# Kernel optimization log

Hardware: AMD Instinct MI355X
Metric: run time of the kernel (lower is better)

## Reference

```python
import jax, jax.numpy as jnp
import numpy as np

B, S, H, C = 8, 4096, 768, 64  # batch, seq_len, hidden_dim, block size


def _xavier(k, shape):
    fan = shape[0] + shape[1]
    return jax.random.normal(k, shape, jnp.float32) * np.sqrt(2.0 / fan)


def setup_inputs() -> dict:
    key = jax.random.key(0)
    kx, kq, kk, kv, k1, k2 = jax.random.split(key, 6)
    return {
        "x": jax.random.normal(kx, (B, S, H), jnp.float32),
        "Wq": _xavier(kq, (H, H)),
        "Wk": _xavier(kk, (H, H)),
        "Wv": _xavier(kv, (H, H)),
        "W1": _xavier(k1, (H, 16)),
        "W2": _xavier(k2, (16, H)),
        "b": jnp.zeros((H,), jnp.float32),
    }


def reference(x, Wq, Wk, Wv, W1, W2, b):
    Bb, Ss, Hh = x.shape
    NB = Ss // C  # number of blocks (seq_len divisible by C, no remainder)
    Q = x @ Wq
    K = x @ Wk
    V = x @ Wv
    # gating alpha: identical every block iteration in the original, compute once
    alpha = jax.nn.sigmoid((x @ W1) @ W2 + b) ** (1.0 / 16.0)  # [B,S,H]
    a = alpha.mean(axis=1, keepdims=True)  # [B,1,H], broadcasts over rows of state
    # blocks to leading axis for scan: [NB, B, C, H]
    qs = Q.reshape(Bb, NB, C, Hh).transpose(1, 0, 2, 3)
    ks = K.reshape(Bb, NB, C, Hh).transpose(1, 0, 2, 3)
    vs = V.reshape(Bb, NB, C, Hh).transpose(1, 0, 2, 3)
    mask = jnp.tril(jnp.ones((C, C), x.dtype))
    scale = 1.0 / np.sqrt(Hh).astype(np.float32)

    def step(St, blk):
        qb, kb, vb = blk  # each [B,C,H]
        # state update first (original updates S before computing output)
        St = St * a + jnp.einsum("bch,bcd->bhd", kb, vb)  # [B,H,H]
        # intra-block: scores masked by MULTIPLICATION (as in original), then softmax
        scores = jnp.einsum("bch,bdh->bcd", qb, kb) * mask * scale
        w = jax.nn.softmax(scores, axis=-1)
        out = jnp.einsum("bch,bhd->bcd", qb, St) + jnp.einsum("bcd,bde->bce", w, vb)
        return St, out

    S0 = jnp.zeros((Bb, Hh, Hh), x.dtype)
    _, outs = jax.lax.scan(step, S0, (qs, ks, vs))  # outs: [NB,B,C,H]
    O = outs.transpose(1, 0, 2, 3).reshape(Bb, Ss, Hh)
    return O
```

## Files before the change

kernel.cpp:

```cpp
#include <hip/hip_runtime.h>

#define B_ 8
#define S_ 4096
#define H_ 768
#define C_ 64
#define NB_ 64
#define M_ (B_*S_)

#define NCH_ 8
#define LCH_ 8

typedef _Float16 f16x8 __attribute__((ext_vector_type(8)));
typedef _Float16 f16x4 __attribute__((ext_vector_type(4)));
typedef float    f32x4 __attribute__((ext_vector_type(4)));

__global__ __launch_bounds__(256) void k_transpose(const float* __restrict__ src,
                                                   _Float16* __restrict__ dst) {
  __shared__ float tile[32][33];
  const int t = threadIdx.x;
  const int tx = t & 31, ty = t >> 5;
  const int n0 = blockIdx.x * 32, k0 = blockIdx.y * 32;
#pragma unroll
  for (int i = 0; i < 4; ++i)
    tile[ty + i*8][tx] = src[(k0 + ty + i*8) * H_ + n0 + tx];
  __syncthreads();
#pragma unroll
  for (int i = 0; i < 4; ++i)
    dst[(n0 + ty + i*8) * H_ + k0 + tx] = (_Float16)tile[tx][ty + i*8];
}

__global__ __launch_bounds__(256) void k_gemm_qkv(
    const float* __restrict__ x,
    const _Float16* __restrict__ WqT, const _Float16* __restrict__ WkT,
    const _Float16* __restrict__ WvT,
    _Float16* __restrict__ Qb,
    _Float16* __restrict__ KT, _Float16* __restrict__ VT) {
  __shared__ _Float16 xs[64][40];
  __shared__ _Float16 ws[3][128][40];
  const int t = threadIdx.x;
  const int m0 = blockIdx.x * 64, n0 = blockIdx.y * 128;
  const int lane = t & 63, wv = t >> 6;
  const int lm = lane & 15, qd = lane >> 4;
  const int sm = t >> 2, sk = (t & 3) * 8;
  const int wn = t >> 1, wk = (t & 1) * 16;

  f32x4 acc[3][4][2];
#pragma unroll
  for (int a = 0; a < 3; ++a)
#pragma unroll
    for (int i = 0; i < 4; ++i)
#pragma unroll
      for (int n = 0; n < 2; ++n)
        acc[a][i][n] = (f32x4){0.f, 0.f, 0.f, 0.f};

  for (int kk = 0; kk < 24; ++kk) {
    const int k0 = kk * 32;
    __syncthreads();
    {
      const f32x4* xp = (const f32x4*)&x[(size_t)(m0 + sm) * H_ + k0 + sk];
      f32x4 f0 = xp[0], f1 = xp[1];
      f16x8 xv;
#pragma unroll
      for (int j = 0; j < 4; ++j) { xv[j] = (_Float16)f0[j]; xv[4 + j] = (_Float16)f1[j]; }
      *(f16x8*)&xs[sm][sk] = xv;
    }
    {
      const f16x8* wp = (const f16x8*)&WqT[(n0 + wn) * H_ + k0 + wk];
      *(f16x8*)&ws[0][wn][wk] = wp[0]; *(f16x8*)&ws[0][wn][wk + 8] = wp[1];
      wp = (const f16x8*)&WkT[(n0 + wn) * H_ + k0 + wk];
      *(f16x8*)&ws[1][wn][wk] = wp[0]; *(f16x8*)&ws[1][wn][wk + 8] = wp[1];
      wp = (const f16x8*)&WvT[(n0 + wn) * H_ + k0 + wk];
      *(f16x8*)&ws[2][wn][wk] = wp[0]; *(f16x8*)&ws[2][wn][wk + 8] = wp[1];
    }
    __syncthreads();
    f16x8 af[4];
#pragma unroll
    for (int i = 0; i < 4; ++i) af[i] = *(f16x8*)&xs[i*16 + lm][qd*8];
#pragma unroll
    for (int a = 0; a < 3; ++a)
#pragma unroll
      for (int n = 0; n < 2; ++n) {
        f16x8 bfr = *(f16x8*)&ws[a][wv*32 + n*16 + lm][qd*8];
#pragma unroll
        for (int i = 0; i < 4; ++i)
          acc[a][i][n] = __builtin_amdgcn_mfma_f32_16x16x32_f16(af[i], bfr, acc[a][i][n], 0, 0, 0);
      }
  }
#pragma unroll
  for (int i = 0; i < 4; ++i)
#pragma unroll
    for (int n = 0; n < 2; ++n) {
      const int ng = n0 + wv*32 + n*16 + lm;
      const int mg0 = m0 + i*16 + qd*4;
      const int bb = mg0 >> 12, ss = mg0 & (S_ - 1);
#pragma unroll
      for (int r = 0; r < 4; ++r)
        Qb[(size_t)(mg0 + r) * H_ + ng] = (_Float16)acc[0][i][n][r];
      f16x4 kp, vp;
#pragma unroll
      for (int r = 0; r < 4; ++r) {
        kp[r] = (_Float16)acc[1][i][n][r];
        vp[r] = (_Float16)acc[2][i][n][r];
      }
      *(f16x4*)&KT[((size_t)bb * H_ + ng) * S_ + ss] = kp;
      *(f16x4*)&VT[((size_t)bb * H_ + ng) * S_ + ss] = vp;
    }
}

__global__ __launch_bounds__(256) void k_tgemm(const float* __restrict__ x,
                                               const float* __restrict__ W1,
                                               float* __restrict__ tbuf) {
  __shared__ float w1s[768 * 16];
  __shared__ float xs[64 * 129];
  const int t = threadIdx.x;
  const int m0 = blockIdx.x * 64;
  for (int i = t; i < 768 * 16 / 4; i += 256)
    ((f32x4*)w1s)[i] = ((const f32x4*)W1)[i];
  const int row = t & 63, cg = t >> 6;
  f32x4 acc = (f32x4){0.f, 0.f, 0.f, 0.f};
  for (int kc = 0; kc < 768; kc += 128) {
    __syncthreads();
    for (int i = 0; i < 32; ++i) {
      const int idx = t + 256 * i;
      const int r = idx >> 7, c = idx & 127;
      xs[r * 129 + c] = x[(size_t)(m0 + r) * H_ + kc + c];
    }
    __syncthreads();
#pragma unroll 8
    for (int kl = 0; kl < 128; ++kl) {
      const float a = xs[row * 129 + kl];
      const f32x4 w = *(const f32x4*)&w1s[(kc + kl) * 16 + cg * 4];
#pragma unroll
      for (int j = 0; j < 4; ++j) acc[j] += a * w[j];
    }
  }
  *(f32x4*)&tbuf[(size_t)(m0 + row) * 16 + cg * 4] = acc;
}

__global__ __launch_bounds__(256) void k_areduce(const float* __restrict__ tbuf,
                                                 const float* __restrict__ W2,
                                                 const float* __restrict__ bias,
                                                 float* __restrict__ abuf) {
  __shared__ float ts[128 * 17];
  __shared__ float rbuf[8 * 32];
  const int t = threadIdx.x;
  const int b = blockIdx.y, hc = blockIdx.x;
  const int hl = t & 31, sg = t >> 5;
  const int h = hc * 32 + hl;
  float w2r[16];
#pragma unroll
  for (int j = 0; j < 16; ++j) w2r[j] = W2[j * H_ + h];
  const float bb = bias[h];
  float asum = 0.f;
  const float* tb = &tbuf[(size_t)(b * S_) * 16];
  for (int sc = 0; sc < S_; sc += 128) {
    __syncthreads();
    for (int i = 0; i < 8; ++i) {
      const int idx = t + 256 * i;
      const int sl = idx >> 4, j = idx & 15;
      ts[sl * 17 + j] = tb[(size_t)(sc + sl) * 16 + j];
    }
    __syncthreads();
    for (int i = 0; i < 16; ++i) {
      const int sl = sg + i * 8;
      float z = bb;
      const float* tr = &ts[sl * 17];
#pragma unroll
      for (int j = 0; j < 16; ++j) z += tr[j] * w2r[j];
      const float sgm = 1.f / (1.f + __expf(-z));
      asum += sqrtf(sqrtf(sqrtf(sqrtf(sgm))));
    }
  }
  rbuf[sg * 32 + hl] = asum;
  __syncthreads();
  if (t < 32) {
    float s = 0.f;
#pragma unroll
    for (int g = 0; g < 8; ++g) s += rbuf[g * 32 + t];
    abuf[b * H_ + hc * 32 + t] = s * (1.f / (float)S_);
  }
}

__global__ __launch_bounds__(256) void k_scores_y(
    const _Float16* __restrict__ Qb, const _Float16* __restrict__ KT,
    const _Float16* __restrict__ VT, float* __restrict__ O) {
  __shared__ float qs[64 * 68];
  __shared__ float ks[64 * 68];
  __shared__ float wb[64 * 68];
  __shared__ float vsb[64 * 68];
  const int t = threadIdx.x;
  const int nb = blockIdx.x, b = blockIdx.y;
  const size_t base = ((size_t)b * S_ + nb * 64) * H_;
  const int tc = t >> 4, td = t & 15;
  const int srow = t >> 2, sseg = (t & 3) * 16;

  float scr[4][4];
#pragma unroll
  for (int i = 0; i < 4; ++i)
#pragma unroll
    for (int u = 0; u < 4; ++u) scr[i][u] = 0.f;

  for (int hc = 0; hc < 12; ++hc) {
    __syncthreads();
    {
      const f16x8* qp = (const f16x8*)&Qb[base + (size_t)srow * H_ + hc * 64 + sseg];
      f16x8 q0 = qp[0], q1 = qp[1];
#pragma unroll
      for (int j = 0; j < 8; ++j) {
        qs[(sseg + j) * 68 + srow] = (float)q0[j];
        qs[(sseg + 8 + j) * 68 + srow] = (float)q1[j];
      }
    }
    {
      const size_t krow = ((size_t)b * H_ + hc * 64 + srow) * S_ + nb * 64 + sseg;
      f16x8 k0 = *(const f16x8*)&KT[krow];
      f16x8 k1 = *(const f16x8*)&KT[krow + 8];
      f32x4 f;
#pragma unroll
      for (int j = 0; j < 4; ++j) f[j] = (float)k0[j];
      *(f32x4*)&ks[srow * 68 + sseg] = f;
#pragma unroll
      for (int j = 0; j < 4; ++j) f[j] = (float)k0[4 + j];
      *(f32x4*)&ks[srow * 68 + sseg + 4] = f;
#pragma unroll
      for (int j = 0; j < 4; ++j) f[j] = (float)k1[j];
      *(f32x4*)&ks[srow * 68 + sseg + 8] = f;
#pragma unroll
      for (int j = 0; j < 4; ++j) f[j] = (float)k1[4 + j];
      *(f32x4*)&ks[srow * 68 + sseg + 12] = f;
    }
    __syncthreads();
#pragma unroll 4
    for (int h = 0; h < 64; ++h) {
      const f32x4 qv = *(f32x4*)&qs[h * 68 + tc * 4];
      const f32x4 kv = *(f32x4*)&ks[h * 68 + td * 4];
#pragma unroll
      for (int i = 0; i < 4; ++i)
#pragma unroll
        for (int u = 0; u < 4; ++u) scr[i][u] += qv[i] * kv[u];
    }
  }
  const float scale = 0.036084391824351615f;
#pragma unroll
  for (int i = 0; i < 4; ++i)
#pragma unroll
    for (int u = 0; u < 4; ++u) {
      const int c = tc * 4 + i, d = td * 4 + u;
      wb[d * 68 + c] = (d <= c) ? scr[i][u] * scale : 0.f;
    }
  __syncthreads();
  {
    const int r = t >> 2, g = t & 3;
    float vals[16];
    float mx = -1e30f;
#pragma unroll
    for (int i = 0; i < 16; ++i) {
      vals[i] = wb[(g * 16 + i) * 68 + r];
      mx = fmaxf(mx, vals[i]);
    }
    mx = fmaxf(mx, __shfl_xor(mx, 1));
    mx = fmaxf(mx, __shfl_xor(mx, 2));
    float sm = 0.f;
#pragma unroll
    for (int i = 0; i < 16; ++i) { vals[i] = __expf(vals[i] - mx); sm += vals[i]; }
    sm += __shfl_xor(sm, 1);
    sm += __shfl_xor(sm, 2);
    const float inv = 1.f / sm;
#pragma unroll
    for (int i = 0; i < 16; ++i) wb[(g * 16 + i) * 68 + r] = vals[i] * inv;
  }
  for (int ec = 0; ec < 12; ++ec) {
    __syncthreads();
    {
      const size_t vrow = ((size_t)b * H_ + ec * 64 + srow) * S_ + nb * 64 + sseg;
      f16x8 v0 = *(const f16x8*)&VT[vrow];
      f16x8 v1 = *(const f16x8*)&VT[vrow + 8];
#pragma unroll
      for (int j = 0; j < 8; ++j) {
        vsb[(sseg + j) * 68 + srow] = (float)v0[j];
        vsb[(sseg + 8 + j) * 68 + srow] = (float)v1[j];
      }
    }
    __syncthreads();
    float y[4][4];
#pragma unroll
    for (int i = 0; i < 4; ++i)
#pragma unroll
      for (int u = 0; u < 4; ++u) y[i][u] = 0.f;
#pragma unroll 4
    for (int j = 0; j < 64; ++j) {
      const f32x4 wv = *(f32x4*)&wb[j * 68 + tc * 4];
      const f32x4 vv = *(f32x4*)&vsb[j * 68 + td * 4];
#pragma unroll
      for (int i = 0; i < 4; ++i)
#pragma unroll
        for (int u = 0; u < 4; ++u) y[i][u] += wv[i] * vv[u];
    }
#pragma unroll
    for (int i = 0; i < 4; ++i) {
      f32x4 yv = {y[i][0], y[i][1], y[i][2], y[i][3]};
      *(f32x4*)&O[base + (size_t)(tc * 4 + i) * H_ + ec * 64 + td * 4] = yv;
    }
  }
}

__global__ __launch_bounds__(256, 2) void k_chunk_gemm(
    const _Float16* __restrict__ KT, const _Float16* __restrict__ VT,
    const float* __restrict__ abuf, _Float16* __restrict__ Tb) {
  __shared__ _Float16 bs[128][40];
  const int t = threadIdx.x;
  const int b = blockIdx.y;
  const int ch = blockIdx.x & 7, tile = blockIdx.x >> 3;
  const int dt = tile / 6, ht = tile % 6;
  const int w = t >> 6, lane = t & 63;
  const int lm = lane & 15, qd = lane >> 4;
  const int d0 = dt * 128 + w * 32;
  const int h0 = ht * 128;
  const int hrow = t >> 1, hseg = (t & 1) * 16;

  float av[2], pw[2];
  av[0] = abuf[b * H_ + d0 + lm];
  av[1] = abuf[b * H_ + d0 + 16 + lm];
  pw[0] = 1.f; pw[1] = 1.f;

  f32x4 acc[2][8];
#pragma unroll
  for (int ds = 0; ds < 2; ++ds)
#pragma unroll
    for (int hh = 0; hh < 8; ++hh) acc[ds][hh] = (f32x4){0.f, 0.f, 0.f, 0.f};

  const size_t ktb = (size_t)b * H_ * S_;
  for (int kk = 15; kk >= 0; --kk) {
    const int sp = ch * 512 + kk * 32;
    __syncthreads();
    {
      const f16x8* kp = (const f16x8*)&KT[ktb + (size_t)(h0 + hrow) * S_ + sp + hseg];
      *(f16x8*)&bs[hrow][hseg] = kp[0];
      *(f16x8*)&bs[hrow][hseg + 8] = kp[1];
    }
    __syncthreads();
    f16x8 va0 = *(const f16x8*)&VT[ktb + (size_t)(d0 + lm) * S_ + sp + qd * 8];
    f16x8 va1 = *(const f16x8*)&VT[ktb + (size_t)(d0 + 16 + lm) * S_ + sp + qd * 8];
    va0 *= (_Float16)pw[0];
    va1 *= (_Float16)pw[1];
#pragma unroll
    for (int hh = 0; hh < 8; ++hh) {
      const f16x8 kf = *(const f16x8*)&bs[hh * 16 + lm][qd * 8];
      acc[0][hh] = __builtin_amdgcn_mfma_f32_16x16x32_f16(va0, kf, acc[0][hh], 0, 0, 0);
      acc[1][hh] = __builtin_amdgcn_mfma_f32_16x16x32_f16(va1, kf, acc[1][hh], 0, 0, 0);
    }
    if (!(kk & 1)) { pw[0] *= av[0]; pw[1] *= av[1]; }
  }
  _Float16* tp = Tb + (size_t)(b * NCH_ + ch) * 768 * 768;
#pragma unroll
  for (int ds = 0; ds < 2; ++ds)
#pragma unroll
    for (int hh = 0; hh < 8; ++hh)
#pragma unroll
      for (int r = 0; r < 4; ++r)
        tp[(size_t)(d0 + ds * 16 + qd * 4 + r) * 768 + h0 + hh * 16 + lm] =
            (_Float16)acc[ds][hh][r];
}

__global__ __launch_bounds__(256) void k_combine(const float* __restrict__ abuf,
                                                 _Float16* __restrict__ Tb) {
  const int gid = blockIdx.x * 256 + threadIdx.x;
  const int hv = gid % 96;
  const int dl = (gid / 96) & 31;
  const int dt = (gid / (96 * 32)) % 24;
  const int b  = gid / (96 * 32 * 24);
  const float ad = abuf[b * H_ + dt * 32 + dl];
  const float a2 = ad * ad, a4 = a2 * a2;
  const float aL = a4 * a4;
  float carry[8];
#pragma unroll
  for (int j = 0; j < 8; ++j) carry[j] = 0.f;
  const size_t chstride = (size_t)24 * 32 * 768;
  _Float16* p = Tb + (size_t)b * NCH_ * chstride + ((size_t)dt * 32 + dl) * 768 + hv * 8;
  for (int ch = 0; ch < NCH_; ++ch, p += chstride) {
    const f16x8 tv = *(const f16x8*)p;
    f16x8 cv;
#pragma unroll
    for (int j = 0; j < 8; ++j) {
      cv[j] = (_Float16)carry[j];
      carry[j] = carry[j] * aL + (float)tv[j];
    }
    *(f16x8*)p = cv;
  }
}

#define STP 776
__global__ __launch_bounds__(256, 2) void k_scan_out(
    const _Float16* __restrict__ Qb, const _Float16* __restrict__ KT,
    const _Float16* __restrict__ VT, const float* __restrict__ abuf,
    const _Float16* __restrict__ Tb, float* __restrict__ O) {
  __shared__ _Float16 StL[32 * STP];
  const int t = threadIdx.x;
  const int lin = blockIdx.x;
  const int xcd = lin & 7, j = lin >> 3;
  const int g = (j / 24) * 8 + xcd;
  const int dt = j % 24;
  const int ch = g & 7, b = g >> 3;
  const int d0 = dt * 32;
  const int w = t >> 6, lane = t & 63;
  const int lm = lane & 15, qd = lane >> 4;

  const float av0 = abuf[b * H_ + d0 + lm];
  const float av1 = abuf[b * H_ + d0 + 16 + lm];

  f32x4 acc[12][2];
  {
    const _Float16* tp = Tb + ((((size_t)b * NCH_ + ch) * 24 + dt) * 32) * 768;
#pragma unroll
    for (int mt = 0; mt < 12; ++mt) {
      const int h = (w * 12 + mt) * 16 + qd * 4;
      const f16x4 c0 = *(const f16x4*)&tp[(size_t)lm * 768 + h];
      const f16x4 c1 = *(const f16x4*)&tp[(size_t)(16 + lm) * 768 + h];
#pragma unroll
      for (int r = 0; r < 4; ++r) {
        acc[mt][0][r] = (float)c0[r];
        acc[mt][1][r] = (float)c1[r];
      }
    }
  }

  const size_t ktb = (size_t)b * H_ * S_;
  const size_t vrow0 = ktb + (size_t)(d0 + lm) * S_;
  const size_t vrow1 = ktb + (size_t)(d0 + 16 + lm) * S_;

  for (int blk = ch * LCH_; blk < ch * LCH_ + LCH_; ++blk) {
    const int s0 = blk * 64;
    f16x8 vf00 = *(const f16x8*)&VT[vrow0 + s0 + qd * 8];
    f16x8 vf01 = *(const f16x8*)&VT[vrow0 + s0 + 32 + qd * 8];
    f16x8 vf10 = *(const f16x8*)&VT[vrow1 + s0 + qd * 8];
    f16x8 vf11 = *(const f16x8*)&VT[vrow1 + s0 + 32 + qd * 8];
#pragma unroll
    for (int mt = 0; mt < 12; ++mt) {
      const size_t arow = ktb + (size_t)((w * 12 + mt) * 16 + lm) * S_ + s0 + qd * 8;
      f16x8 a0 = *(const f16x8*)&KT[arow];
      f16x8 a1 = *(const f16x8*)&KT[arow + 32];
      f32x4 c0 = acc[mt][0] * av0;
      f32x4 c1 = acc[mt][1] * av1;
      c0 = __builtin_amdgcn_mfma_f32_16x16x32_f16(a0, vf00, c0, 0, 0, 0);
      c0 = __builtin_amdgcn_mfma_f32_16x16x32_f16(a1, vf01, c0, 0, 0, 0);
      c1 = __builtin_amdgcn_mfma_f32_16x16x32_f16(a0, vf10, c1, 0, 0, 0);
      c1 = __builtin_amdgcn_mfma_f32_16x16x32_f16(a1, vf11, c1, 0, 0, 0);
      acc[mt][0] = c0;
      acc[mt][1] = c1;
    }
    __syncthreads();
#pragma unroll
    for (int mt = 0; mt < 12; ++mt) {
      const int h = (w * 12 + mt) * 16 + qd * 4;
      f16x4 p0, p1;
#pragma unroll
      for (int r = 0; r < 4; ++r) {
        p0[r] = (_Float16)acc[mt][0][r];
        p1[r] = (_Float16)acc[mt][1][r];
      }
      *(f16x4*)&StL[lm * STP + h] = p0;
      *(f16x4*)&StL[(16 + lm) * STP + h] = p1;
    }
    __syncthreads();
    f32x4 o0a = {0.f,0.f,0.f,0.f}, o0b = {0.f,0.f,0.f,0.f};
    f32x4 o1a = {0.f,0.f,0.f,0.f}, o1b = {0.f,0.f,0.f,0.f};
    const size_t qrow = ((size_t)b * S_ + s0 + w * 16 + lm) * H_ + qd * 8;
#pragma unroll 3
    for (int kt = 0; kt < 24; kt += 2) {
      f16x8 qa = *(const f16x8*)&Qb[qrow + kt * 32];
      f16x8 qb2 = *(const f16x8*)&Qb[qrow + kt * 32 + 32];
      f16x8 s00 = *(f16x8*)&StL[lm * STP + kt * 32 + qd * 8];
      f16x8 s01 = *(f16x8*)&StL[(16 + lm) * STP + kt * 32 + qd * 8];
      f16x8 s10 = *(f16x8*)&StL[lm * STP + kt * 32 + 32 + qd * 8];
      f16x8 s11 = *(f16x8*)&StL[(16 + lm) * STP + kt * 32 + 32 + qd * 8];
      o0a = __builtin_amdgcn_mfma_f32_16x16x32_f16(qa, s00, o0a, 0, 0, 0);
      o1a = __builtin_amdgcn_mfma_f32_16x16x32_f16(qa, s01, o1a, 0, 0, 0);
      o0b = __builtin_amdgcn_mfma_f32_16x16x32_f16(qb2, s10, o0b, 0, 0, 0);
      o1b = __builtin_amdgcn_mfma_f32_16x16x32_f16(qb2, s11, o1b, 0, 0, 0);
    }
    const f32x4 o0 = o0a + o0b;
    const f32x4 o1 = o1a + o1b;
    const size_t orow = ((size_t)b * S_ + s0 + w * 16 + qd * 4) * H_ + d0;
#pragma unroll
    for (int r = 0; r < 4; ++r) {
      O[orow + (size_t)r * H_ + lm] += o0[r];
      O[orow + (size_t)r * H_ + 16 + lm] += o1[r];
    }
  }
}

extern "C" void kernel_launch(void* const* d_in, const int* in_sizes, int n_in,
                              void* d_out, int out_size, void* d_ws, size_t ws_size,
                              hipStream_t stream) {
  (void)in_sizes; (void)n_in; (void)out_size; (void)ws_size;
  const float* x    = (const float*)d_in[0];
  const float* Wq   = (const float*)d_in[1];
  const float* Wk   = (const float*)d_in[2];
  const float* Wv   = (const float*)d_in[3];
  const float* W1   = (const float*)d_in[4];
  const float* W2   = (const float*)d_in[5];
  const float* bias = (const float*)d_in[6];
  float* O = (float*)d_out;

  char* ws = (char*)d_ws;
  _Float16* Qb  = (_Float16*)ws;
  _Float16* KT  = Qb + (size_t)M_ * H_;
  _Float16* VT  = KT + (size_t)M_ * H_;
  _Float16* WqT = VT + (size_t)M_ * H_;
  _Float16* WkT = WqT + H_ * H_;
  _Float16* WvT = WkT + H_ * H_;
  float* tbuf = (float*)(WvT + H_ * H_);
  float* abuf = tbuf + (size_t)M_ * 16;
  _Float16* Tb = (_Float16*)(abuf + B_ * H_);

  k_transpose<<<dim3(24, 24), 256, 0, stream>>>(Wq, WqT);
  k_transpose<<<dim3(24, 24), 256, 0, stream>>>(Wk, WkT);
  k_transpose<<<dim3(24, 24), 256, 0, stream>>>(Wv, WvT);
  k_tgemm<<<dim3(512), 256, 0, stream>>>(x, W1, tbuf);
  k_areduce<<<dim3(24, 8), 256, 0, stream>>>(tbuf, W2, bias, abuf);
  k_gemm_qkv<<<dim3(512, 6), 256, 0, stream>>>(x, WqT, WkT, WvT, Qb, KT, VT);
  k_scores_y<<<dim3(64, 8), 256, 0, stream>>>(Qb, KT, VT, O);
  k_chunk_gemm<<<dim3(288, 8), 256, 0, stream>>>(KT, VT, abuf, Tb);
  k_combine<<<dim3(2304), 256, 0, stream>>>(abuf, Tb);
  k_scan_out<<<dim3(1536), 256, 0, stream>>>(Qb, KT, VT, abuf, Tb, O);
}
```

Measured before the change: 1.290 ms.

## Rewrite intra-block scores and softmax-V product with MFMA, add row-major K copy

The intra-block attention kernel now uses 16x16x32 f16 MFMA instructions for both QK^T and P·V instead of scalar fp32 FMA loops over shared-memory tiles. Fragments are read directly from global memory, and the softmax probabilities are staged in LDS as f16. To give the QK^T fragment loads a row-major layout, the QKV GEMM also writes an extra row-major K buffer. The cost is an additional M×H f16 write and larger workspace use, plus f16 rounding of the softmax weights.

```diff
diff --git a/kernel.cpp b/kernel.cpp
--- a/kernel.cpp
+++ b/kernel.cpp
@@ -33,7 +33,7 @@
     const float* __restrict__ x,
     const _Float16* __restrict__ WqT, const _Float16* __restrict__ WkT,
     const _Float16* __restrict__ WvT,
-    _Float16* __restrict__ Qb,
+    _Float16* __restrict__ Qb, _Float16* __restrict__ Kb,
     _Float16* __restrict__ KT, _Float16* __restrict__ VT) {
   __shared__ _Float16 xs[64][40];
   __shared__ _Float16 ws[3][128][40];
@@ -94,8 +94,10 @@
       const int mg0 = m0 + i*16 + qd*4;
       const int bb = mg0 >> 12, ss = mg0 & (S_ - 1);
 #pragma unroll
-      for (int r = 0; r < 4; ++r)
+      for (int r = 0; r < 4; ++r) {
         Qb[(size_t)(mg0 + r) * H_ + ng] = (_Float16)acc[0][i][n][r];
+        Kb[(size_t)(mg0 + r) * H_ + ng] = (_Float16)acc[1][i][n][r];
+      }
       f16x4 kp, vp;
 #pragma unroll
       for (int r = 0; r < 4; ++r) {
@@ -181,73 +183,40 @@
   }
 }
 
-__global__ __launch_bounds__(256) void k_scores_y(
-    const _Float16* __restrict__ Qb, const _Float16* __restrict__ KT,
+__global__ __launch_bounds__(256, 2) void k_scores_y(
+    const _Float16* __restrict__ Qb, const _Float16* __restrict__ Kb,
     const _Float16* __restrict__ VT, float* __restrict__ O) {
-  __shared__ float qs[64 * 68];
-  __shared__ float ks[64 * 68];
   __shared__ float wb[64 * 68];
-  __shared__ float vsb[64 * 68];
+  __shared__ __align__(16) _Float16 pl[64 * 72];
   const int t = threadIdx.x;
   const int nb = blockIdx.x, b = blockIdx.y;
-  const size_t base = ((size_t)b * S_ + nb * 64) * H_;
-  const int tc = t >> 4, td = t & 15;
-  const int srow = t >> 2, sseg = (t & 3) * 16;
-
-  float scr[4][4];
-#pragma unroll
-  for (int i = 0; i < 4; ++i)
-#pragma unroll
-    for (int u = 0; u < 4; ++u) scr[i][u] = 0.f;
-
-  for (int hc = 0; hc < 12; ++hc) {
-    __syncthreads();
-    {
-      const f16x8* qp = (const f16x8*)&Qb[base + (size_t)srow * H_ + hc * 64 + sseg];
-      f16x8 q0 = qp[0], q1 = qp[1];
-#pragma unroll
-      for (int j = 0; j < 8; ++j) {
-        qs[(sseg + j) * 68 + srow] = (float)q0[j];
-        qs[(sseg + 8 + j) * 68 + srow] = (float)q1[j];
-      }
-    }
-    {
-      const size_t krow = ((size_t)b * H_ + hc * 64 + srow) * S_ + nb * 64 + sseg;
-      f16x8 k0 = *(const f16x8*)&KT[krow];
-      f16x8 k1 = *(const f16x8*)&KT[krow + 8];
-      f32x4 f;
-#pragma unroll
-      for (int j = 0; j < 4; ++j) f[j] = (float)k0[j];
-      *(f32x4*)&ks[srow * 68 + sseg] = f;
-#pragma unroll
-      for (int j = 0; j < 4; ++j) f[j] = (float)k0[4 + j];
-      *(f32x4*)&ks[srow * 68 + sseg + 4] = f;
-#pragma unroll
-      for (int j = 0; j < 4; ++j) f[j] = (float)k1[j];
-      *(f32x4*)&ks[srow * 68 + sseg + 8] = f;
-#pragma unroll
-      for (int j = 0; j < 4; ++j) f[j] = (float)k1[4 + j];
-      *(f32x4*)&ks[srow * 68 + sseg + 12] = f;
-    }
-    __syncthreads();
-#pragma unroll 4
-    for (int h = 0; h < 64; ++h) {
-      const f32x4 qv = *(f32x4*)&qs[h * 68 + tc * 4];
-      const f32x4 kv = *(f32x4*)&ks[h * 68 + td * 4];
-#pragma unroll
-      for (int i = 0; i < 4; ++i)
-#pragma unroll
-        for (int u = 0; u < 4; ++u) scr[i][u] += qv[i] * kv[u];
+  const int w = t >> 6, lane = t & 63;
+  const int lm = lane & 15, qd = lane >> 4;
+  const size_t rbase = (size_t)b * S_ + (size_t)nb * 64;
+
+  f32x4 sacc[4];
+#pragma unroll
+  for (int u = 0; u < 4; ++u) sacc[u] = (f32x4){0.f, 0.f, 0.f, 0.f};
+  for (int hk = 0; hk < 24; ++hk) {
+    const f16x8 qa = *(const f16x8*)&Qb[(rbase + w * 16 + lm) * H_ + hk * 32 + qd * 8];
+#pragma unroll
+    for (int u = 0; u < 4; ++u) {
+      const f16x8 kb = *(const f16x8*)&Kb[(rbase + u * 16 + lm) * H_ + hk * 32 + qd * 8];
+      sacc[u] = __builtin_amdgcn_mfma_f32_16x16x32_f16(qa, kb, sacc[u], 0, 0, 0);
     }
   }
   const float scale = 0.036084391824351615f;
 #pragma unroll
-  for (int i = 0; i < 4; ++i)
-#pragma unroll
-    for (int u = 0; u < 4; ++u) {
-      const int c = tc * 4 + i, d = td * 4 + u;
-      wb[d * 68 + c] = (d <= c) ? scr[i][u] * scale : 0.f;
-    }
+  for (int u = 0; u < 4; ++u) {
+    const int cp = u * 16 + lm;
+    f32x4 m;
+#pragma unroll
+    for (int r = 0; r < 4; ++r) {
+      const int c = w * 16 + qd * 4 + r;
+      m[r] = (cp <= c) ? sacc[u][r] * scale : 0.f;
+    }
+    *(f32x4*)&wb[cp * 68 + w * 16 + qd * 4] = m;
+  }
   __syncthreads();
   {
     const int r = t >> 2, g = t & 3;
@@ -267,41 +236,37 @@
     sm += __shfl_xor(sm, 2);
     const float inv = 1.f / sm;
 #pragma unroll
-    for (int i = 0; i < 16; ++i) wb[(g * 16 + i) * 68 + r] = vals[i] * inv;
-  }
-  for (int ec = 0; ec < 12; ++ec) {
-    __syncthreads();
-    {
-      const size_t vrow = ((size_t)b * H_ + ec * 64 + srow) * S_ + nb * 64 + sseg;
-      f16x8 v0 = *(const f16x8*)&VT[vrow];
-      f16x8 v1 = *(const f16x8*)&VT[vrow + 8];
-#pragma unroll
-      for (int j = 0; j < 8; ++j) {
-        vsb[(sseg + j) * 68 + srow] = (float)v0[j];
-        vsb[(sseg + 8 + j) * 68 + srow] = (float)v1[j];
-      }
-    }
-    __syncthreads();
-    float y[4][4];
+    for (int i = 0; i < 16; ++i)
+      pl[r * 72 + g * 16 + i] = (_Float16)(vals[i] * inv);
+  }
+  __syncthreads();
+  f32x4 acc[4][12];
+#pragma unroll
+  for (int i = 0; i < 4; ++i)
+#pragma unroll
+    for (int nd = 0; nd < 12; ++nd) acc[i][nd] = (f32x4){0.f, 0.f, 0.f, 0.f};
+#pragma unroll
+  for (int kk = 0; kk < 2; ++kk) {
+    f16x8 sa[4];
 #pragma unroll
     for (int i = 0; i < 4; ++i)
-#pragma unroll
-      for (int u = 0; u < 4; ++u) y[i][u] = 0.f;
-#pragma unroll 4
-    for (int j = 0; j < 64; ++j) {
-      const f32x4 wv = *(f32x4*)&wb[j * 68 + tc * 4];
-      const f32x4 vv = *(f32x4*)&vsb[j * 68 + td * 4];
+      sa[i] = *(const f16x8*)&pl[(i * 16 + lm) * 72 + kk * 32 + qd * 8];
+#pragma unroll
+    for (int nd = 0; nd < 12; ++nd) {
+      const f16x8 vb = *(const f16x8*)&VT[((size_t)b * H_ + w * 192 + nd * 16 + lm) * S_
+                                          + nb * 64 + kk * 32 + qd * 8];
 #pragma unroll
       for (int i = 0; i < 4; ++i)
-#pragma unroll
-        for (int u = 0; u < 4; ++u) y[i][u] += wv[i] * vv[u];
-    }
-#pragma unroll
-    for (int i = 0; i < 4; ++i) {
-      f32x4 yv = {y[i][0], y[i][1], y[i][2], y[i][3]};
-      *(f32x4*)&O[base + (size_t)(tc * 4 + i) * H_ + ec * 64 + td * 4] = yv;
-    }
-  }
+        acc[i][nd] = __builtin_amdgcn_mfma_f32_16x16x32_f16(sa[i], vb, acc[i][nd], 0, 0, 0);
+    }
+  }
+#pragma unroll
+  for (int i = 0; i < 4; ++i)
+#pragma unroll
+    for (int nd = 0; nd < 12; ++nd)
+#pragma unroll
+      for (int r = 0; r < 4; ++r)
+        O[(rbase + i * 16 + qd * 4 + r) * H_ + w * 192 + nd * 16 + lm] = acc[i][nd][r];
 }
 
 __global__ __launch_bounds__(256, 2) void k_chunk_gemm(
@@ -504,7 +469,8 @@
 
   char* ws = (char*)d_ws;
   _Float16* Qb  = (_Float16*)ws;
-  _Float16* KT  = Qb + (size_t)M_ * H_;
+  _Float16* Kb  = Qb + (size_t)M_ * H_;
+  _Float16* KT  = Kb + (size_t)M_ * H_;
   _Float16* VT  = KT + (size_t)M_ * H_;
   _Float16* WqT = VT + (size_t)M_ * H_;
   _Float16* WkT = WqT + H_ * H_;
@@ -518,8 +484,8 @@
   k_transpose<<<dim3(24, 24), 256, 0, stream>>>(Wv, WvT);
   k_tgemm<<<dim3(512), 256, 0, stream>>>(x, W1, tbuf);
   k_areduce<<<dim3(24, 8), 256, 0, stream>>>(tbuf, W2, bias, abuf);
-  k_gemm_qkv<<<dim3(512, 6), 256, 0, stream>>>(x, WqT, WkT, WvT, Qb, KT, VT);
-  k_scores_y<<<dim3(64, 8), 256, 0, stream>>>(Qb, KT, VT, O);
+  k_gemm_qkv<<<dim3(512, 6), 256, 0, stream>>>(x, WqT, WkT, WvT, Qb, Kb, KT, VT);
+  k_scores_y<<<dim3(64, 8), 256, 0, stream>>>(Qb, Kb, VT, O);
   k_chunk_gemm<<<dim3(288, 8), 256, 0, stream>>>(KT, VT, abuf, Tb);
   k_combine<<<dim3(2304), 256, 0, stream>>>(abuf, Tb);
   k_scan_out<<<dim3(1536), 256, 0, stream>>>(Qb, KT, VT, abuf, Tb, O);
```

Result: no change. 1.273 ms (-1.3%).
